# Optimization experiments

Hardware: AMD Instinct MI355X
Metric: run time of the kernel (lower is better)

Reference implementation:

```python
import jax, jax.numpy as jnp
import numpy as np

DIM = 4096
HEADS = 32
HD = DIM // HEADS  # 128
SEQ = 2048
BSZ = 2
ALEN = 10
ROPE_THETA = 10000.0


def _make_freqs(seq, hd):
    inv = 1.0 / (ROPE_THETA ** (np.arange(0, hd, 2, dtype=np.float32) / hd))
    t = np.arange(seq, dtype=np.float32)
    ang = np.outer(t, inv)  # [seq, hd/2]
    return jnp.asarray(np.cos(ang)), jnp.asarray(np.sin(ang))


def setup_inputs() -> dict:
    key = jax.random.key(0)
    ks = jax.random.split(key, 8)
    s = 1.0 / np.sqrt(DIM)
    x = jax.random.normal(ks[0], (BSZ, SEQ, DIM), jnp.float32)
    wq = jax.random.normal(ks[1], (DIM, DIM), jnp.float32) * s  # [in, out]
    wk = jax.random.normal(ks[2], (DIM, DIM), jnp.float32) * s
    wv = jax.random.normal(ks[3], (DIM, DIM), jnp.float32) * s
    wo = jax.random.normal(ks[4], (DIM, DIM), jnp.float32) * s
    gate = 0.1 * jax.random.normal(ks[5], (1, HEADS, 1, 1), jnp.float32)
    adapter = jax.random.normal(ks[6], (1, ALEN, DIM), jnp.float32)
    freqs_cos, freqs_sin = _make_freqs(SEQ, HD)
    # causal additive mask, start_pos = 0
    mask = jnp.triu(jnp.full((1, 1, SEQ, SEQ), -1e9, jnp.float32), k=1)
    return {"x": x, "wq": wq, "wk": wk, "wv": wv, "wo": wo, "gate": gate,
            "adapter": adapter, "freqs_cos": freqs_cos, "freqs_sin": freqs_sin,
            "mask": mask, "start_pos": 0, "random_init": 0}


def _rope(t, cos, sin):
    # t: [b, s, H, hd]; cos/sin: [s, hd/2] -> broadcast (1, s, 1, hd/2)
    b, s, h, hd = t.shape
    t2 = t.reshape(b, s, h, hd // 2, 2)
    tr, ti = t2[..., 0], t2[..., 1]
    c = cos[None, :, None, :]
    sn = sin[None, :, None, :]
    orr = tr * c - ti * sn
    oi = tr * sn + ti * c
    return jnp.stack([orr, oi], axis=-1).reshape(b, s, h, hd)


def reference(x, wq, wk, wv, wo, gate, adapter, freqs_cos, freqs_sin, mask,
              start_pos, random_init):
    bsz, seqlen, dim = x.shape
    hd = 2 * freqs_cos.shape[-1]
    H = dim // hd
    L = adapter.shape[1]
    scale = 1.0 / jnp.sqrt(jnp.float32(hd))

    xq = (x @ wq).reshape(bsz, seqlen, H, hd)
    xk = (x @ wk).reshape(bsz, seqlen, H, hd)
    xv = (x @ wv).reshape(bsz, seqlen, H, hd)

    xq = _rope(xq, freqs_cos, freqs_sin)
    xk = _rope(xk, freqs_cos, freqs_sin)

    # adapter prefix K/V (no RoPE), shared across batch
    ak = (adapter @ wk).reshape(1, L, H, hd)  # [1, L, H, hd]
    av = (adapter @ wv).reshape(1, L, H, hd)

    # scores: normal keys masked causally; adapter keys unmasked (extra zeros)
    scores_n = jnp.einsum('bqhd,bkhd->bhqk', xq, xk) * scale + mask
    scores_a = jnp.einsum('bqhd,lhd->bhql', xq, ak[0]) * scale

    if random_init:
        # joint softmax over [adapter | normal] keys
        sc = jax.nn.softmax(jnp.concatenate([scores_a, scores_n], axis=-1), axis=-1)
        pa, pn = sc[..., :L], sc[..., L:]
    else:
        pa = jnp.tanh(gate) * jax.nn.softmax(scores_a, axis=-1)
        pn = jax.nn.softmax(scores_n, axis=-1)

    out = (jnp.einsum('bhql,lhd->bqhd', pa, av[0])
           + jnp.einsum('bhqk,bkhd->bqhd', pn, xv))
    out = out.reshape(bsz, seqlen, H * hd)
    return out @ wo
```

## Files before the change

### kernel.cpp

```cpp
#include <hip/hip_runtime.h>
#include <hip/hip_bf16.h>
#include <cstdint>

typedef float  f32x4  __attribute__((ext_vector_type(4)));
typedef __bf16 bf16x8 __attribute__((ext_vector_type(8)));
typedef __bf16 bf16x4 __attribute__((ext_vector_type(4)));
typedef __bf16 bf16x2 __attribute__((ext_vector_type(2)));

#define AS1 __attribute__((address_space(1)))
#define AS3 __attribute__((address_space(3)))

static constexpr int D   = 4096;
static constexpr int SEQ = 2048;
static constexpr int MX  = 4224;

__device__ __forceinline__ void gload_lds16(const void* g, void* l) {
  __builtin_amdgcn_global_load_lds((AS1 void*)(g), (AS3 void*)(l), 16, 0, 0);
}

__device__ __forceinline__ f32x4 mfma16(bf16x8 a, bf16x8 b, f32x4 c) {
  return __builtin_amdgcn_mfma_f32_16x16x32_bf16(a, b, c, 0, 0, 0);
}

__device__ __forceinline__ int xcd_chunk(int orig, int nwg) {
  int q = nwg >> 3, r = nwg & 7;
  int xcd = orig & 7, pos = orig >> 3;
  return (xcd < r ? xcd * (q + 1) : r * (q + 1) + (xcd - r) * q) + pos;
}

#define BARF() asm volatile("s_barrier" ::: "memory")

__global__ __launch_bounds__(256) void transpose_cast4(const float* __restrict__ w0,
                                                       const float* __restrict__ w1,
                                                       const float* __restrict__ w2,
                                                       const float* __restrict__ w3,
                                                       __bf16* __restrict__ WT) {
  __shared__ float tile[64][65];
  const float* W = (blockIdx.z == 0) ? w0 : (blockIdx.z == 1) ? w1
                 : (blockIdx.z == 2) ? w2 : w3;
  __bf16* dst = WT + (size_t)blockIdx.z * D * D;
  const int t  = threadIdx.x;
  const int r0 = blockIdx.x * 64;
  const int c0 = blockIdx.y * 64;
#pragma unroll
  for (int p = 0; p < 4; ++p) {
    int e = p * 1024 + t * 4;
    int row = e >> 6, col = e & 63;
    f32x4 v = *(const f32x4*)(W + (size_t)(r0 + row) * D + c0 + col);
#pragma unroll
    for (int i = 0; i < 4; ++i) tile[row][col + i] = v[i];
  }
  __syncthreads();
#pragma unroll
  for (int p = 0; p < 2; ++p) {
    int e = p * 2048 + t * 8;
    int orow = e >> 6, ocol = e & 63;
    bf16x8 o;
#pragma unroll
    for (int i = 0; i < 8; ++i) o[i] = (__bf16)tile[ocol + i][orow];
    *(bf16x8*)(dst + (size_t)(c0 + orow) * D + r0 + ocol) = o;
  }
}

__global__ __launch_bounds__(256) void build_xa(const float* __restrict__ x,
                                                const float* __restrict__ ad,
                                                __bf16* __restrict__ xa) {
  int idx = blockIdx.x * 256 + threadIdx.x;
  int e = idx * 4;
  int row = e >> 12, col = e & 4095;
  f32x4 v = {};
  if (row < 4096)      v = *(const f32x4*)(x + (size_t)row * D + col);
  else if (row < 4106) v = *(const f32x4*)(ad + (size_t)(row - 4096) * D + col);
  bf16x4 o;
#pragma unroll
  for (int i = 0; i < 4; ++i) o[i] = (__bf16)v[i];
  *(bf16x4*)(xa + (size_t)row * D + col) = o;
}

template <int MODE>
__global__ __launch_bounds__(512, 2) void gemm256(const __bf16* __restrict__ A,
                                                  const __bf16* __restrict__ BT,
                                                  void* __restrict__ O0,
                                                  void* __restrict__ O1,
                                                  void* __restrict__ O2,
                                                  const float* __restrict__ FC,
                                                  const float* __restrict__ FS,
                                                  int Mt) {
  __shared__ __bf16 lds[65536];
  const int tid = threadIdx.x;
  const int wv = tid >> 6, ln = tid & 63;
  const int lg = ln >> 4, lr = ln & 15;

  const int nwg = gridDim.x;
  const int wgid = xcd_chunk(blockIdx.x, nwg);
  const int m0 = (wgid % Mt) * 256;
  const int n0 = (wgid / Mt) * 256;
  const int wm = (wv >> 2) * 128, wn = (wv & 3) * 64;

  auto stageHalf = [&](int k, int mat, int half) {
    const int slot = k & 1;
    const int kt = k * 64;
    const __bf16* base = mat ? BT + (size_t)(n0 + half * 128) * 4096
                             : A  + (size_t)(m0 + half * 128) * 4096;
#pragma unroll
    for (int i = 0; i < 2; ++i) {
      int c = i * 512 + tid;
      int r = c >> 3;
      int ch = (c & 7) ^ (r & 7);
      gload_lds16(base + (size_t)r * 4096 + kt + ch * 8,
                  lds + slot * 32768 + mat * 16384 + half * 8192 +
                      (i * 512 + wv * 64) * 8);
    }
  };

  f32x4 acc[8][4] = {};
  bf16x8 aLo[4][2], aHi[4][2], bLo[2][2], bHi[2][2];

  auto rdA = [&](const __bf16* pA, int mi, int kk) -> bf16x8 {
    int r = wm + mi * 16 + lr;
    int R = r & 127;
    int cw = (kk * 4 + lg) ^ (R & 7);
    return *(const bf16x8*)(pA + (r >> 7) * 8192 + R * 64 + cw * 8);
  };
  auto rdB = [&](const __bf16* pB, int ni, int kk) -> bf16x8 {
    int n = wn + ni * 16 + lr;
    int R = n & 127;
    int cw = (kk * 4 + lg) ^ (R & 7);
    return *(const bf16x8*)(pB + (n >> 7) * 8192 + R * 64 + cw * 8);
  };

  stageHalf(0, 0, 0);
  stageHalf(0, 1, 0);
  stageHalf(0, 0, 1);
  stageHalf(0, 1, 1);
  stageHalf(1, 0, 0);
  stageHalf(1, 1, 0);

  for (int k = 0; k < 63; ++k) {
    const int slot = k & 1;
    const __bf16* pA = lds + slot * 32768;
    const __bf16* pB = lds + slot * 32768 + 16384;

    stageHalf(k + 1, 0, 1);
    asm volatile("s_waitcnt vmcnt(8)" ::: "memory");
    BARF();
#pragma unroll
    for (int mi = 0; mi < 4; ++mi)
#pragma unroll
      for (int kk = 0; kk < 2; ++kk) aLo[mi][kk] = rdA(pA, mi, kk);
#pragma unroll
    for (int ni = 0; ni < 2; ++ni)
#pragma unroll
      for (int kk = 0; kk < 2; ++kk) bLo[ni][kk] = rdB(pB, ni, kk);
    __builtin_amdgcn_s_setprio(1);
#pragma unroll
    for (int kk = 0; kk < 2; ++kk)
#pragma unroll
      for (int mi = 0; mi < 4; ++mi)
#pragma unroll
        for (int ni = 0; ni < 2; ++ni)
          acc[mi][ni] = mfma16(aLo[mi][kk], bLo[ni][kk], acc[mi][ni]);
    __builtin_amdgcn_s_setprio(0);
    BARF();

    stageHalf(k + 1, 1, 1);
#pragma unroll
    for (int mi = 0; mi < 4; ++mi)
#pragma unroll
      for (int kk = 0; kk < 2; ++kk) aHi[mi][kk] = rdA(pA, mi + 4, kk);
    asm volatile("s_waitcnt vmcnt(8)" ::: "memory");
    BARF();
    __builtin_amdgcn_s_setprio(1);
#pragma unroll
    for (int kk = 0; kk < 2; ++kk)
#pragma unroll
      for (int mi = 0; mi < 4; ++mi)
#pragma unroll
        for (int ni = 0; ni < 2; ++ni)
          acc[mi + 4][ni] = mfma16(aHi[mi][kk], bLo[ni][kk], acc[mi + 4][ni]);
    __builtin_amdgcn_s_setprio(0);
    BARF();

    if (k + 2 < 64) stageHalf(k + 2, 0, 0);
#pragma unroll
    for (int ni = 0; ni < 2; ++ni)
#pragma unroll
      for (int kk = 0; kk < 2; ++kk) bHi[ni][kk] = rdB(pB, ni + 2, kk);
    BARF();
    __builtin_amdgcn_s_setprio(1);
#pragma unroll
    for (int kk = 0; kk < 2; ++kk)
#pragma unroll
      for (int mi = 0; mi < 4; ++mi)
#pragma unroll
        for (int ni = 0; ni < 2; ++ni)
          acc[mi + 4][ni + 2] = mfma16(aHi[mi][kk], bHi[ni][kk], acc[mi + 4][ni + 2]);
    __builtin_amdgcn_s_setprio(0);
    BARF();

    if (k + 2 < 64) stageHalf(k + 2, 1, 0);
    BARF();
    __builtin_amdgcn_s_setprio(1);
#pragma unroll
    for (int kk = 0; kk < 2; ++kk)
#pragma unroll
      for (int mi = 0; mi < 4; ++mi)
#pragma unroll
        for (int ni = 0; ni < 2; ++ni)
          acc[mi][ni + 2] = mfma16(aLo[mi][kk], bHi[ni][kk], acc[mi][ni + 2]);
    __builtin_amdgcn_s_setprio(0);
    BARF();
  }

  {
    const __bf16* pA = lds + (63 & 1) * 32768;
    const __bf16* pB = lds + (63 & 1) * 32768 + 16384;
    asm volatile("s_waitcnt vmcnt(0)" ::: "memory");
    BARF();
#pragma unroll
    for (int mi = 0; mi < 4; ++mi)
#pragma unroll
      for (int kk = 0; kk < 2; ++kk) aLo[mi][kk] = rdA(pA, mi, kk);
#pragma unroll
    for (int ni = 0; ni < 2; ++ni)
#pragma unroll
      for (int kk = 0; kk < 2; ++kk) bLo[ni][kk] = rdB(pB, ni, kk);
#pragma unroll
    for (int kk = 0; kk < 2; ++kk)
#pragma unroll
      for (int mi = 0; mi < 4; ++mi)
#pragma unroll
        for (int ni = 0; ni < 2; ++ni)
          acc[mi][ni] = mfma16(aLo[mi][kk], bLo[ni][kk], acc[mi][ni]);
#pragma unroll
    for (int mi = 0; mi < 4; ++mi)
#pragma unroll
      for (int kk = 0; kk < 2; ++kk) aHi[mi][kk] = rdA(pA, mi + 4, kk);
#pragma unroll
    for (int ni = 0; ni < 2; ++ni)
#pragma unroll
      for (int kk = 0; kk < 2; ++kk) bHi[ni][kk] = rdB(pB, ni + 2, kk);
#pragma unroll
    for (int kk = 0; kk < 2; ++kk)
#pragma unroll
      for (int mi = 0; mi < 4; ++mi)
#pragma unroll
        for (int ni = 0; ni < 2; ++ni) {
          acc[mi + 4][ni]     = mfma16(aHi[mi][kk], bLo[ni][kk], acc[mi + 4][ni]);
          acc[mi + 4][ni + 2] = mfma16(aHi[mi][kk], bHi[ni][kk], acc[mi + 4][ni + 2]);
          acc[mi][ni + 2]     = mfma16(aLo[mi][kk], bHi[ni][kk], acc[mi][ni + 2]);
        }
  }

  if constexpr (MODE == 0) {
    const int sel = n0 >> 12;
    const int colb = n0 & 4095;
    if (sel < 2) {
      __bf16* out = sel ? (__bf16*)O1 : (__bf16*)O0;
#pragma unroll
      for (int mi = 0; mi < 8; ++mi)
#pragma unroll
        for (int j = 0; j < 4; ++j) {
          int row = m0 + wm + mi * 16 + lg * 4 + j;
          int s = row & (SEQ - 1);
#pragma unroll
          for (int ni = 0; ni < 4; ++ni) {
            int col = colb + wn + ni * 16 + lr;
            int fi = (col & 127) >> 1;
            float c  = FC[s * 64 + fi];
            float sn = FS[s * 64 + fi];
            float v = acc[mi][ni][j];
            float p = __shfl_xor(v, 1);
            float o = (lr & 1) ? (p * sn + v * c) : (v * c - p * sn);
            out[(size_t)row * 4096 + col] = (__bf16)o;
          }
        }
    } else {
      __bf16* vT = (__bf16*)O2;
#pragma unroll
      for (int mi = 0; mi < 8; ++mi) {
        int row0 = m0 + wm + mi * 16 + lg * 4;
#pragma unroll
        for (int ni = 0; ni < 4; ++ni) {
          int col = colb + wn + ni * 16 + lr;
          bf16x4 pk;
#pragma unroll
          for (int j = 0; j < 4; ++j) pk[j] = (__bf16)acc[mi][ni][j];
          *(bf16x4*)(vT + (size_t)col * MX + row0) = pk;
        }
      }
    }
  } else {
    float* out = (float*)O0;
#pragma unroll
    for (int mi = 0; mi < 8; ++mi)
#pragma unroll
      for (int ni = 0; ni < 4; ++ni)
#pragma unroll
        for (int j = 0; j < 4; ++j) {
          int row = m0 + wm + mi * 16 + lg * 4 + j;
          int col = n0 + wn + ni * 16 + lr;
          out[(size_t)row * 4096 + col] = acc[mi][ni][j];
        }
  }
}

__global__ __launch_bounds__(256) void gemm_adapter(const __bf16* __restrict__ xa,
                                                    const __bf16* __restrict__ BT,
                                                    __bf16* __restrict__ kb,
                                                    __bf16* __restrict__ vT) {
  const int tid = threadIdx.x;
  const int wv = tid >> 6, ln = tid & 63;
  const int lg = ln >> 4, lr = ln & 15;
  const int col0 = blockIdx.x * 256 + wv * 64;
  f32x4 acc[4] = {};
  for (int kt = 0; kt < 4096; kt += 32) {
    bf16x8 a = *(const bf16x8*)(xa + (size_t)(4096 + lr) * 4096 + kt + lg * 8);
#pragma unroll
    for (int ni = 0; ni < 4; ++ni) {
      bf16x8 b = *(const bf16x8*)(BT + (size_t)(col0 + ni * 16 + lr) * 4096 +
                                  kt + lg * 8);
      acc[ni] = mfma16(a, b, acc[ni]);
    }
  }
#pragma unroll
  for (int ni = 0; ni < 4; ++ni)
#pragma unroll
    for (int j = 0; j < 4; ++j) {
      int row = 4096 + lg * 4 + j;
      int col = col0 + ni * 16 + lr;
      if (col < 4096) kb[(size_t)row * 4096 + col] = (__bf16)acc[ni][j];
      else            vT[(size_t)(col & 4095) * MX + row] = (__bf16)acc[ni][j];
    }
}

__global__ __launch_bounds__(256) void attn_kernel(const __bf16* __restrict__ Q,
                                                   const __bf16* __restrict__ K,
                                                   const __bf16* __restrict__ VT,
                                                   const float* __restrict__ gate,
                                                   __bf16* __restrict__ Out) {
  __shared__ __bf16 Ks[2][64 * 128];
  __shared__ __bf16 Vs[2][128 * 64];
  __shared__ __bf16 Ps[4][32 * 64];

  const int tid = threadIdx.x;
  const int wv = tid >> 6, ln = tid & 63;
  const int lg = ln >> 4, lr = ln & 15;

  const int wgid = xcd_chunk(blockIdx.x, 512);
  const int px = wgid & 7;
  const int hb = wgid >> 3;
  const int h = hb & 31, b = hb >> 5;

  const float scale = 0.08838834764831845f;
  const float g = tanhf(gate[h]);

  auto stage = [&](int t, int buf) {
    const int kv0 = t * 64;
#pragma unroll
    for (int j = 0; j < 4; ++j) {
      int c = wv * 256 + j * 64 + ln;
      int rk = c >> 4, sck = (c & 15) ^ (rk & 7);
      gload_lds16(K + (size_t)(b * SEQ + kv0 + rk) * D + h * 128 + sck * 8,
                  Ks[buf] + (wv * 256 + j * 64) * 8);
      int rv = c >> 3, scv = (c & 7) ^ (rv & 7);
      gload_lds16(VT + (size_t)(h * 128 + rv) * MX + b * SEQ + kv0 + scv * 8,
                  Vs[buf] + (wv * 256 + j * 64) * 8);
    }
  };

  auto run_supertile = [&](int qt) {
    const int q0 = qt * 128;
    const int qbase = b * SEQ + q0 + wv * 32;

    bf16x8 qf[2][4];
#pragma unroll
    for (int mi = 0; mi < 2; ++mi)
#pragma unroll
      for (int kd = 0; kd < 4; ++kd)
        qf[mi][kd] = *(const bf16x8*)(Q + (size_t)(qbase + mi * 16 + lr) * D +
                                      h * 128 + kd * 32 + lg * 8);

    f32x4 O[2][8] = {};
    float mI2[2], lI2[2];
#pragma unroll
    for (int mi = 0; mi < 2; ++mi) { mI2[mi] = -1e30f; lI2[mi] = 0.f; }

    const int ntiles = 2 * qt + 2;
    stage(0, 0);

    for (int t = 0; t < ntiles; ++t) {
      const int cur = t & 1;
      const int kv0 = t * 64;
      if (t + 1 < ntiles) {
        stage(t + 1, cur ^ 1);
        asm volatile("s_waitcnt vmcnt(8)" ::: "memory");
      } else {
        asm volatile("s_waitcnt vmcnt(0)" ::: "memory");
      }
      __builtin_amdgcn_s_barrier();
      __builtin_amdgcn_sched_barrier(0);

      f32x4 S[2][4] = {};
      __builtin_amdgcn_s_setprio(1);
#pragma unroll
      for (int kd = 0; kd < 4; ++kd) {
        bf16x8 kf[4];
#pragma unroll
        for (int nf = 0; nf < 4; ++nf) {
          int kr = nf * 16 + lr;
          kf[nf] = *(const bf16x8*)(Ks[cur] + kr * 128 +
                                    (((kd * 4 + lg) ^ (kr & 7)) * 8));
        }
#pragma unroll
        for (int mi = 0; mi < 2; ++mi)
#pragma unroll
          for (int nf = 0; nf < 4; ++nf)
            S[mi][nf] = mfma16(kf[nf], qf[mi][kd], S[mi][nf]);
      }
      __builtin_amdgcn_s_setprio(0);

      float r2[2]; int grew = 0;
#pragma unroll
      for (int mi = 0; mi < 2; ++mi) {
        const int qg = q0 + wv * 32 + mi * 16 + lr;
        float mo = mI2[mi];
        float mt = -3e38f;
#pragma unroll
        for (int nf = 0; nf < 4; ++nf)
#pragma unroll
          for (int j = 0; j < 4; ++j) {
            int kvg = kv0 + nf * 16 + lg * 4 + j;
            float s = S[mi][nf][j] * scale;
            s = (kvg > qg) ? -1e30f : s;
            S[mi][nf][j] = s;
            mt = fmaxf(mt, s);
          }
        mt = fmaxf(mt, __shfl_xor(mt, 16));
        mt = fmaxf(mt, __shfl_xor(mt, 32));
        float mn = fmaxf(mo, mt);
        float ps = 0.f;
#pragma unroll
        for (int nf = 0; nf < 4; ++nf)
#pragma unroll
          for (int j = 0; j < 4; ++j) {
            float p = __expf(S[mi][nf][j] - mn);
            S[mi][nf][j] = p;
            ps += p;
          }
        ps += __shfl_xor(ps, 16);
        ps += __shfl_xor(ps, 32);
        float r = __expf(mo - mn);
        lI2[mi] = lI2[mi] * r + ps;
        mI2[mi] = mn;
        r2[mi] = r;
        grew |= (mn > mo) ? 1 : 0;
      }
      if (__any(grew)) {
#pragma unroll
        for (int mi = 0; mi < 2; ++mi)
#pragma unroll
          for (int j = 0; j < 4; ++j) {
            float rj = __shfl(r2[mi], lg * 4 + j);
#pragma unroll
            for (int n = 0; n < 8; ++n) O[mi][n][j] *= rj;
          }
      }

#pragma unroll
      for (int mi = 0; mi < 2; ++mi) {
        int q = mi * 16 + lr;
#pragma unroll
        for (int nf = 0; nf < 4; ++nf) {
          int kv = nf * 16 + lg * 4;
          bf16x4 pk;
#pragma unroll
          for (int j = 0; j < 4; ++j) pk[j] = (__bf16)S[mi][nf][j];
          *(bf16x4*)(Ps[wv] + q * 64 + (((kv >> 3) ^ (q & 7)) * 8) + (kv & 7)) = pk;
        }
      }

      __builtin_amdgcn_s_setprio(1);
#pragma unroll
      for (int kkv = 0; kkv < 2; ++kkv) {
        bf16x8 pf[2];
#pragma unroll
        for (int mi = 0; mi < 2; ++mi) {
          int prw = mi * 16 + lr;
          pf[mi] = *(const bf16x8*)(Ps[wv] + prw * 64 +
                                    (((kkv * 4 + lg) ^ (prw & 7)) * 8));
        }
#pragma unroll
        for (int n = 0; n < 8; ++n) {
          int vr = n * 16 + lr;
          bf16x8 vf = *(const bf16x8*)(Vs[cur] + vr * 64 +
                                       (((kkv * 4 + lg) ^ (vr & 7)) * 8));
#pragma unroll
          for (int mi = 0; mi < 2; ++mi) O[mi][n] = mfma16(pf[mi], vf, O[mi][n]);
        }
      }
      __builtin_amdgcn_s_setprio(0);

      __builtin_amdgcn_s_barrier();
      __builtin_amdgcn_sched_barrier(0);
    }

#pragma unroll
    for (int mi = 0; mi < 2; ++mi) {
      float inv = 1.0f / lI2[mi];
#pragma unroll
      for (int j = 0; j < 4; ++j) {
        float invj = __shfl(inv, lg * 4 + j);
#pragma unroll
        for (int n = 0; n < 8; ++n) O[mi][n][j] *= invj;
      }
    }

    {
      f32x4 Sa[2] = {};
#pragma unroll
      for (int kd = 0; kd < 4; ++kd) {
        bf16x8 kfa = *(const bf16x8*)(K + (size_t)(2 * SEQ + lr) * D +
                                      h * 128 + kd * 32 + lg * 8);
#pragma unroll
        for (int mi = 0; mi < 2; ++mi) Sa[mi] = mfma16(kfa, qf[mi][kd], Sa[mi]);
      }
#pragma unroll
      for (int mi = 0; mi < 2; ++mi) {
        float mt = -3e38f;
#pragma unroll
        for (int j = 0; j < 4; ++j) {
          int kv = lg * 4 + j;
          float s = Sa[mi][j] * scale;
          s = (kv >= 10) ? -1e30f : s;
          Sa[mi][j] = s;
          mt = fmaxf(mt, s);
        }
        mt = fmaxf(mt, __shfl_xor(mt, 16));
        mt = fmaxf(mt, __shfl_xor(mt, 32));
        float ps = 0.f;
#pragma unroll
        for (int j = 0; j < 4; ++j) {
          float p = __expf(Sa[mi][j] - mt);
          Sa[mi][j] = p;
          ps += p;
        }
        ps += __shfl_xor(ps, 16);
        ps += __shfl_xor(ps, 32);
        float gs = g / ps;
        int q = mi * 16 + lr;
        int kv = lg * 4;
        bf16x4 pk, z = {};
#pragma unroll
        for (int j = 0; j < 4; ++j) pk[j] = (__bf16)(Sa[mi][j] * gs);
        *(bf16x4*)(Ps[wv] + q * 64 + (((kv >> 3) ^ (q & 7)) * 8) + (kv & 7)) = pk;
        int kv2 = 16 + kv;
        *(bf16x4*)(Ps[wv] + q * 64 + (((kv2 >> 3) ^ (q & 7)) * 8) + (kv2 & 7)) = z;
      }
      bf16x8 pfa[2];
#pragma unroll
      for (int mi = 0; mi < 2; ++mi) {
        int prw = mi * 16 + lr;
        pfa[mi] = *(const bf16x8*)(Ps[wv] + prw * 64 + ((lg ^ (prw & 7)) * 8));
      }
#pragma unroll
      for (int n = 0; n < 8; ++n) {
        bf16x8 vfa = *(const bf16x8*)(VT + (size_t)(h * 128 + n * 16 + lr) * MX +
                                      2 * SEQ + lg * 8);
#pragma unroll
        for (int mi = 0; mi < 2; ++mi) O[mi][n] = mfma16(pfa[mi], vfa, O[mi][n]);
      }
    }

#pragma unroll
    for (int mi = 0; mi < 2; ++mi)
#pragma unroll
      for (int n = 0; n < 8; ++n)
#pragma unroll
        for (int j = 0; j < 4; ++j)
          Out[(size_t)(qbase + mi * 16 + lg * 4 + j) * D + h * 128 + n * 16 + lr] =
              (__bf16)O[mi][n][j];
  };

  run_supertile(15 - px);
  run_supertile(px);
}

extern "C" void kernel_launch(void* const* d_in, const int* in_sizes, int n_in,
                              void* d_out, int out_size, void* d_ws, size_t ws_size,
                              hipStream_t stream) {
  const float* x    = (const float*)d_in[0];
  const float* wq   = (const float*)d_in[1];
  const float* wk   = (const float*)d_in[2];
  const float* wv   = (const float*)d_in[3];
  const float* wo   = (const float*)d_in[4];
  const float* gate = (const float*)d_in[5];
  const float* ad   = (const float*)d_in[6];
  const float* fc   = (const float*)d_in[7];
  const float* fs   = (const float*)d_in[8];

  const size_t WSZ = (size_t)D * D * 2;
  const size_t XSZ = (size_t)MX * D * 2;
  if (ws_size < 4 * WSZ + XSZ + WSZ + 3 * XSZ) return;

  char* w = (char*)d_ws;
  size_t off = 0;
  auto alloc = [&](size_t sz) { void* p = w + off; off += sz; return p; };
  __bf16* wqT = (__bf16*)alloc(WSZ);
  __bf16* wkT = (__bf16*)alloc(WSZ);
  __bf16* wvT = (__bf16*)alloc(WSZ);
  __bf16* woT = (__bf16*)alloc(WSZ);
  __bf16* xa  = (__bf16*)alloc(XSZ);
  __bf16* qb  = (__bf16*)alloc(WSZ);
  __bf16* kb  = (__bf16*)alloc(XSZ);
  __bf16* vb  = (__bf16*)alloc(XSZ);
  __bf16* vT  = (__bf16*)alloc(XSZ);
  __bf16* attn = vb;
  (void)wkT; (void)wvT;

  dim3 blk(256);
  transpose_cast4<<<dim3(64, 64, 4), blk, 0, stream>>>(wq, wk, wv, wo, wqT);
  build_xa<<<dim3(16896), blk, 0, stream>>>(x, ad, xa);

  gemm256<0><<<dim3(16 * 48), dim3(512), 0, stream>>>(xa, wqT, qb, kb, vT,
                                                      fc, fs, 16);
  gemm_adapter<<<dim3(32), blk, 0, stream>>>(xa, wkT, kb, vT);

  attn_kernel<<<dim3(512), blk, 0, stream>>>(qb, kb, vT, gate, attn);

  gemm256<1><<<dim3(16 * 16), dim3(512), 0, stream>>>(attn, woT, d_out,
                                                      nullptr, nullptr,
                                                      nullptr, nullptr, 16);
}
```

Before: 824.1 us.

## Restructure GEMM main loop into two phases with all fragment loads up front

```diff
diff --git a/kernel.cpp b/kernel.cpp
--- a/kernel.cpp
+++ b/kernel.cpp
@@ -136,22 +136,32 @@
   stageHalf(1, 0, 0);
   stageHalf(1, 1, 0);
 
-  for (int k = 0; k < 63; ++k) {
+  for (int k = 0; k < 64; ++k) {
     const int slot = k & 1;
     const __bf16* pA = lds + slot * 32768;
     const __bf16* pB = lds + slot * 32768 + 16384;
 
-    stageHalf(k + 1, 0, 1);
-    asm volatile("s_waitcnt vmcnt(8)" ::: "memory");
+    if (k + 1 < 64) stageHalf(k + 1, 0, 1);
+    if (k < 63) asm volatile("s_waitcnt vmcnt(6)" ::: "memory");
+    else        asm volatile("s_waitcnt vmcnt(0)" ::: "memory");
     BARF();
+    __builtin_amdgcn_sched_barrier(0);
+
 #pragma unroll
     for (int mi = 0; mi < 4; ++mi)
 #pragma unroll
-      for (int kk = 0; kk < 2; ++kk) aLo[mi][kk] = rdA(pA, mi, kk);
+      for (int kk = 0; kk < 2; ++kk) {
+        aLo[mi][kk] = rdA(pA, mi, kk);
+        aHi[mi][kk] = rdA(pA, mi + 4, kk);
+      }
 #pragma unroll
     for (int ni = 0; ni < 2; ++ni)
 #pragma unroll
-      for (int kk = 0; kk < 2; ++kk) bLo[ni][kk] = rdB(pB, ni, kk);
+      for (int kk = 0; kk < 2; ++kk) {
+        bLo[ni][kk] = rdB(pB, ni, kk);
+        bHi[ni][kk] = rdB(pB, ni + 2, kk);
+      }
+
     __builtin_amdgcn_s_setprio(1);
 #pragma unroll
     for (int kk = 0; kk < 2; ++kk)
@@ -161,15 +171,14 @@
         for (int ni = 0; ni < 2; ++ni)
           acc[mi][ni] = mfma16(aLo[mi][kk], bLo[ni][kk], acc[mi][ni]);
     __builtin_amdgcn_s_setprio(0);
+
     BARF();
-
-    stageHalf(k + 1, 1, 1);
-#pragma unroll
-    for (int mi = 0; mi < 4; ++mi)
-#pragma unroll
-      for (int kk = 0; kk < 2; ++kk) aHi[mi][kk] = rdA(pA, mi + 4, kk);
-    asm volatile("s_waitcnt vmcnt(8)" ::: "memory");
-    BARF();
+    __builtin_amdgcn_sched_barrier(0);
+
+    if (k + 1 < 64) stageHalf(k + 1, 1, 1);
+    if (k + 2 < 64) { stageHalf(k + 2, 0, 0);
+                      stageHalf(k + 2, 1, 0); }
+
     __builtin_amdgcn_s_setprio(1);
 #pragma unroll
     for (int kk = 0; kk < 2; ++kk)
@@ -178,16 +187,6 @@
 #pragma unroll
         for (int ni = 0; ni < 2; ++ni)
           acc[mi + 4][ni] = mfma16(aHi[mi][kk], bLo[ni][kk], acc[mi + 4][ni]);
-    __builtin_amdgcn_s_setprio(0);
-    BARF();
-
-    if (k + 2 < 64) stageHalf(k + 2, 0, 0);
-#pragma unroll
-    for (int ni = 0; ni < 2; ++ni)
-#pragma unroll
-      for (int kk = 0; kk < 2; ++kk) bHi[ni][kk] = rdB(pB, ni + 2, kk);
-    BARF();
-    __builtin_amdgcn_s_setprio(1);
 #pragma unroll
     for (int kk = 0; kk < 2; ++kk)
 #pragma unroll
@@ -195,12 +194,6 @@
 #pragma unroll
         for (int ni = 0; ni < 2; ++ni)
           acc[mi + 4][ni + 2] = mfma16(aHi[mi][kk], bHi[ni][kk], acc[mi + 4][ni + 2]);
-    __builtin_amdgcn_s_setprio(0);
-    BARF();
-
-    if (k + 2 < 64) stageHalf(k + 2, 1, 0);
-    BARF();
-    __builtin_amdgcn_s_setprio(1);
 #pragma unroll
     for (int kk = 0; kk < 2; ++kk)
 #pragma unroll
@@ -209,47 +202,9 @@
         for (int ni = 0; ni < 2; ++ni)
           acc[mi][ni + 2] = mfma16(aLo[mi][kk], bHi[ni][kk], acc[mi][ni + 2]);
     __builtin_amdgcn_s_setprio(0);
+
     BARF();
-  }
-
-  {
-    const __bf16* pA = lds + (63 & 1) * 32768;
-    const __bf16* pB = lds + (63 & 1) * 32768 + 16384;
-    asm volatile("s_waitcnt vmcnt(0)" ::: "memory");
-    BARF();
-#pragma unroll
-    for (int mi = 0; mi < 4; ++mi)
-#pragma unroll
-      for (int kk = 0; kk < 2; ++kk) aLo[mi][kk] = rdA(pA, mi, kk);
-#pragma unroll
-    for (int ni = 0; ni < 2; ++ni)
-#pragma unroll
-      for (int kk = 0; kk < 2; ++kk) bLo[ni][kk] = rdB(pB, ni, kk);
-#pragma unroll
-    for (int kk = 0; kk < 2; ++kk)
-#pragma unroll
-      for (int mi = 0; mi < 4; ++mi)
-#pragma unroll
-        for (int ni = 0; ni < 2; ++ni)
-          acc[mi][ni] = mfma16(aLo[mi][kk], bLo[ni][kk], acc[mi][ni]);
-#pragma unroll
-    for (int mi = 0; mi < 4; ++mi)
-#pragma unroll
-      for (int kk = 0; kk < 2; ++kk) aHi[mi][kk] = rdA(pA, mi + 4, kk);
-#pragma unroll
-    for (int ni = 0; ni < 2; ++ni)
-#pragma unroll
-      for (int kk = 0; kk < 2; ++kk) bHi[ni][kk] = rdB(pB, ni + 2, kk);
-#pragma unroll
-    for (int kk = 0; kk < 2; ++kk)
-#pragma unroll
-      for (int mi = 0; mi < 4; ++mi)
-#pragma unroll
-        for (int ni = 0; ni < 2; ++ni) {
-          acc[mi + 4][ni]     = mfma16(aHi[mi][kk], bLo[ni][kk], acc[mi + 4][ni]);
-          acc[mi + 4][ni + 2] = mfma16(aHi[mi][kk], bHi[ni][kk], acc[mi + 4][ni + 2]);
-          acc[mi][ni + 2]     = mfma16(aLo[mi][kk], bHi[ni][kk], acc[mi][ni + 2]);
-        }
+    __builtin_amdgcn_sched_barrier(0);
   }
 
   if constexpr (MODE == 0) {
@@ -616,7 +571,7 @@
   __bf16* vb  = (__bf16*)alloc(XSZ);
   __bf16* vT  = (__bf16*)alloc(XSZ);
   __bf16* attn = vb;
-  (void)wkT; (void)wvT;
+  (void)wvT;
 
   dim3 blk(256);
   transpose_cast4<<<dim3(64, 64, 4), blk, 0, stream>>>(wq, wk, wv, wo, wqT);
```

Measured after the change: 834.2 us. About the same (+1.2%).
